# Kernel tuning notes

Hardware: AMD Instinct MI355X
Metric: run time of the kernel (lower is better)

The kernel has to match this reference:

```python
import jax, jax.numpy as jnp
import numpy as np

N = 50000      # total nodes
E = 800000     # total edges (avg degree 16)
D = 64         # in_node_feats = in_edge_feats = out_feats


def setup_inputs() -> dict:
    key = jax.random.key(0)
    ks = jax.random.split(key, 9)
    node_feats = jax.random.normal(ks[0], (N, D), dtype=jnp.float32)
    edge_feats = jax.random.normal(ks[1], (E, D), dtype=jnp.float32)
    src = jax.random.randint(ks[2], (E,), 0, N)
    dst = jax.random.randint(ks[3], (E,), 0, N)
    # in-degree per node (clipped to >=1 to avoid div-by-zero, matching a valid graph)
    deg = jnp.maximum(jax.ops.segment_sum(jnp.ones((E,), jnp.float32), dst, num_segments=N), 1.0)
    degs = deg[:, None]                                   # (N, 1)
    norm = (1.0 / jnp.sqrt(deg[src] * deg[dst]))[:, None]  # (E, 1)
    s = 1.0 / np.sqrt(D)
    Wn = jax.random.uniform(ks[4], (D, D), jnp.float32, -s, s)
    bn = jax.random.uniform(ks[5], (D,), jnp.float32, -s, s)
    We = jax.random.uniform(ks[6], (D, D), jnp.float32, -s, s)
    be = jax.random.uniform(ks[7], (D,), jnp.float32, -s, s)
    res_w = jax.random.normal(ks[8], (1, D), jnp.float32)  # nn.Embedding(1, out_feats).weight
    return {"node_feats": node_feats, "edge_feats": edge_feats, "degs": degs,
            "norm": norm, "src": src, "dst": dst,
            "Wn": Wn, "bn": bn, "We": We, "be": be, "res_w": res_w}


def reference(node_feats, edge_feats, degs, norm, src, dst, Wn, bn, We, be, res_w):
    h = node_feats @ Wn.T + bn                      # (N, D) projected node feats
    ep = edge_feats @ We.T + be                     # (E, D) projected edge feats
    # copy_u gather + relu + norm scale on edges
    m = norm * jax.nn.relu(h[src] + ep)             # (E, D)
    # copy_e + sum scatter-reduction to destination nodes
    agg = jax.ops.segment_sum(m, dst, num_segments=N)  # (N, D)
    # residual branch
    res = jax.nn.relu(h + res_w) / degs             # (N, D), degs broadcasts over D
    return agg + res
```

## Files before the change

kernel.cpp:

```cpp
#include <hip/hip_runtime.h>

#define N_NODES 50000
#define N_EDGES 800000
#define BR 128
#define BRN 64
#define MAXDEG 64
#define NODE_BLOCKS ((N_NODES + BRN - 1) / BRN)
#define ZERO_BLOCKS ((N_NODES + 255) / 256)

using bf16x8 = __attribute__((ext_vector_type(8))) short;
using f32x4  = __attribute__((ext_vector_type(4))) float;

__device__ __forceinline__ unsigned int cvt_pk_bf16(float lo, float hi) {
    unsigned int r;
    asm("v_cvt_pk_bf16_f32 %0, %1, %2" : "=v"(r) : "v"(lo), "v"(hi));
    return r;
}

__device__ __forceinline__ float f4c(const float4 v, int n) {
    switch (n) { case 0: return v.x; case 1: return v.y; case 2: return v.z; default: return v.w; }
}

#define ASWZ(k4, r) (((((r) >> 2) ^ ((k4) & 7)) << 2) | ((r) & 3))

__global__ __launch_bounds__(256) void node_kernel(
    const float* __restrict__ nf, const float* __restrict__ Wn,
    const float* __restrict__ bn, float* __restrict__ h_out,
    const float* __restrict__ We, uint4* __restrict__ Wbe,
    int* __restrict__ cursor) {
    __shared__ float Ast[64][64];
    __shared__ float Ws[64][64];
    const int t = threadIdx.x;
    const int bid = blockIdx.x;

    if (bid >= NODE_BLOCKS) {
        int xb = bid - NODE_BLOCKS;
        if (xb < ZERO_BLOCKS) {
            int i = xb * 256 + t;
            if (i < N_NODES) cursor[i] = 0;
        } else {
#pragma unroll
            for (int i = 0; i < 2; ++i) {
                int task = t + i * 256;
                int frag = task >> 6, lane = task & 63;
                int s = frag >> 2, n = frag & 3;
                int c = 4 * (lane & 15) + n;
                int kb = s * 32 + ((lane >> 4) << 3);
                const float* wp = We + c * 64 + kb;
                float4 a = *(const float4*)wp;
                float4 b = *(const float4*)(wp + 4);
                uint4 o;
                o.x = cvt_pk_bf16(a.x, a.y);
                o.y = cvt_pk_bf16(a.z, a.w);
                o.z = cvt_pk_bf16(b.x, b.y);
                o.w = cvt_pk_bf16(b.z, b.w);
                Wbe[task] = o;
            }
        }
        return;
    }

    const int row0 = bid * BRN;

#pragma unroll
    for (int i = 0; i < 4; ++i) {
        int task = t + i * 256;
        int r = task >> 4;
        int k4 = task & 15;
        int grow = row0 + r;
        float4 v = make_float4(0.f, 0.f, 0.f, 0.f);
        if (grow < N_NODES) v = *(const float4*)(nf + (size_t)grow * 64 + k4 * 4);
        int sc = ASWZ(k4, r);
        Ast[k4 * 4 + 0][sc] = v.x;
        Ast[k4 * 4 + 1][sc] = v.y;
        Ast[k4 * 4 + 2][sc] = v.z;
        Ast[k4 * 4 + 3][sc] = v.w;
    }
#pragma unroll
    for (int i = 0; i < 4; ++i) {
        int task = t + i * 256;
        int c = task & 63;
        int k4 = task >> 6;
        float4 v = *(const float4*)(Wn + c * 64 + k4 * 4);
        Ws[k4 * 4 + 0][c] = v.x;
        Ws[k4 * 4 + 1][c] = v.y;
        Ws[k4 * 4 + 2][c] = v.z;
        Ws[k4 * 4 + 3][c] = v.w;
    }
    __syncthreads();

    const int tx = t & 15, ty = t >> 4;
    const int ca = ty * 4;
    const int cb = tx * 4;

    float acc[4][4];
#pragma unroll
    for (int r = 0; r < 4; ++r)
#pragma unroll
        for (int c = 0; c < 4; ++c) acc[r][c] = 0.f;

#pragma unroll 16
    for (int k = 0; k < 64; ++k) {
        const int f = (k >> 2) & 7;
        float4 w = *(float4*)&Ws[k][cb];
        float4 a = *(float4*)&Ast[k][(ty ^ f) << 2];
        float ar[4] = {a.x, a.y, a.z, a.w};
#pragma unroll
        for (int r = 0; r < 4; ++r) {
            acc[r][0] = fmaf(ar[r], w.x, acc[r][0]);
            acc[r][1] = fmaf(ar[r], w.y, acc[r][1]);
            acc[r][2] = fmaf(ar[r], w.z, acc[r][2]);
            acc[r][3] = fmaf(ar[r], w.w, acc[r][3]);
        }
    }

    float4 b4 = *(const float4*)(bn + cb);
#pragma unroll
    for (int r = 0; r < 4; ++r) {
        int grow = row0 + ca + r;
        if (grow < N_NODES) {
            float4 h4;
            h4.x = acc[r][0] + b4.x;
            h4.y = acc[r][1] + b4.y;
            h4.z = acc[r][2] + b4.z;
            h4.w = acc[r][3] + b4.w;
            *(float4*)(h_out + (size_t)grow * 64 + cb) = h4;
        }
    }
}

__global__ __launch_bounds__(256, 4) void edge_kernel(
    const float* __restrict__ ef, const uint4* __restrict__ Wbe,
    const float* __restrict__ be,
    const int* __restrict__ dst, const float* __restrict__ norm,
    const int* __restrict__ src, int* __restrict__ cursor,
    const float* __restrict__ h, unsigned short* __restrict__ mbuf) {
    __shared__ int slot_l[BR];
    __shared__ float nrm_l[BR];

    const int t = threadIdx.x;
    const int e0 = blockIdx.x * BR;
    const int w = t >> 6, l = t & 63;
    const int l15 = l & 15, lg = l >> 4;
    const int r0base = w * 32;

    if (t < BR) {
        nrm_l[t] = norm[e0 + t];
        int d = dst[e0 + t];
        int rank = atomicAdd(&cursor[d], 1);
        slot_l[t] = (rank < MAXDEG) ? (d * MAXDEG + rank) : -1;
    }

    float4 araw[2][4];
#pragma unroll
    for (int mt = 0; mt < 2; ++mt) {
        const float* rp = ef + (size_t)(e0 + r0base + mt * 16 + l15) * 64 + lg * 8;
        araw[mt][0] = *(const float4*)(rp);
        araw[mt][1] = *(const float4*)(rp + 4);
        araw[mt][2] = *(const float4*)(rp + 32);
        araw[mt][3] = *(const float4*)(rp + 36);
    }
    bf16x8 bfrag[2][4];
#pragma unroll
    for (int s = 0; s < 2; ++s)
#pragma unroll
        for (int n = 0; n < 4; ++n) {
            union { uint4 u; bf16x8 v; } cv;
            cv.u = Wbe[(s * 4 + n) * 64 + l];
            bfrag[s][n] = cv.v;
        }
    float4 hv[2][4];
#pragma unroll
    for (int mt = 0; mt < 2; ++mt)
#pragma unroll
        for (int r = 0; r < 4; ++r) {
            int sn = src[e0 + r0base + mt * 16 + lg * 4 + r];
            hv[mt][r] = *(const float4*)(h + (size_t)sn * 64 + 4 * l15);
        }
    float4 bev4 = *(const float4*)(be + 4 * l15);

    __builtin_amdgcn_sched_barrier(0);

    bf16x8 afrag[2][2];
#pragma unroll
    for (int mt = 0; mt < 2; ++mt)
#pragma unroll
        for (int s = 0; s < 2; ++s) {
            float4 x = araw[mt][s * 2];
            float4 y = araw[mt][s * 2 + 1];
            union { uint4 u; bf16x8 v; } cv;
            cv.u.x = cvt_pk_bf16(x.x, x.y);
            cv.u.y = cvt_pk_bf16(x.z, x.w);
            cv.u.z = cvt_pk_bf16(y.x, y.y);
            cv.u.w = cvt_pk_bf16(y.z, y.w);
            afrag[mt][s] = cv.v;
        }

    f32x4 acc[2][4];
#pragma unroll
    for (int mt = 0; mt < 2; ++mt)
#pragma unroll
        for (int n = 0; n < 4; ++n) acc[mt][n] = (f32x4){0.f, 0.f, 0.f, 0.f};

#pragma unroll
    for (int mt = 0; mt < 2; ++mt)
#pragma unroll
        for (int n = 0; n < 4; ++n)
#pragma unroll
            for (int s = 0; s < 2; ++s)
                acc[mt][n] = __builtin_amdgcn_mfma_f32_16x16x32_bf16(
                    afrag[mt][s], bfrag[s][n], acc[mt][n], 0, 0, 0);

    __syncthreads();

#pragma unroll
    for (int mt = 0; mt < 2; ++mt) {
#pragma unroll
        for (int r = 0; r < 4; ++r) {
            int row = r0base + mt * 16 + lg * 4 + r;
            float nm = nrm_l[row];
            float m0 = nm * fmaxf(f4c(hv[mt][r], 0) + acc[mt][0][r] + bev4.x, 0.f);
            float m1 = nm * fmaxf(f4c(hv[mt][r], 1) + acc[mt][1][r] + bev4.y, 0.f);
            float m2 = nm * fmaxf(f4c(hv[mt][r], 2) + acc[mt][2][r] + bev4.z, 0.f);
            float m3 = nm * fmaxf(f4c(hv[mt][r], 3) + acc[mt][3][r] + bev4.w, 0.f);
            uint2 pk;
            pk.x = cvt_pk_bf16(m0, m1);
            pk.y = cvt_pk_bf16(m2, m3);
            int slot = slot_l[row];
            if (slot >= 0)
                *(uint2*)(mbuf + (size_t)slot * 64 + 4 * l15) = pk;
        }
    }
}

__global__ __launch_bounds__(256, 8) void reduce_kernel(
    const unsigned short* __restrict__ mbuf, const int* __restrict__ cnts,
    const float* __restrict__ h, const float* __restrict__ degs,
    const float* __restrict__ resw, float* __restrict__ out) {
    const int t = threadIdx.x;
    const int n = blockIdx.x * 16 + (t >> 4);
    if (n >= N_NODES) return;
    const int q = t & 15;

    float4 hq = *(const float4*)(h + (size_t)n * 64 + 4 * q);
    float4 rw = *(const float4*)(resw + 4 * q);
    float invd = 1.0f / degs[n];
    int cnt = cnts[n];
    if (cnt > MAXDEG) cnt = MAXDEG;

    const uint2* mp = (const uint2*)mbuf + (size_t)n * MAXDEG * 16 + q;
    float a0 = 0.f, a1 = 0.f, a2 = 0.f, a3 = 0.f;
    float b0 = 0.f, b1 = 0.f, b2 = 0.f, b3 = 0.f;
    int i = 0;
    for (; i + 1 < cnt; i += 2) {
        uint2 va = mp[(size_t)i * 16];
        uint2 vb = mp[(size_t)(i + 1) * 16];
        a0 += __uint_as_float(va.x << 16);
        a1 += __uint_as_float(va.x & 0xffff0000u);
        a2 += __uint_as_float(va.y << 16);
        a3 += __uint_as_float(va.y & 0xffff0000u);
        b0 += __uint_as_float(vb.x << 16);
        b1 += __uint_as_float(vb.x & 0xffff0000u);
        b2 += __uint_as_float(vb.y << 16);
        b3 += __uint_as_float(vb.y & 0xffff0000u);
    }
    if (i < cnt) {
        uint2 v = mp[(size_t)i * 16];
        a0 += __uint_as_float(v.x << 16);
        a1 += __uint_as_float(v.x & 0xffff0000u);
        a2 += __uint_as_float(v.y << 16);
        a3 += __uint_as_float(v.y & 0xffff0000u);
    }
    float4 o;
    o.x = fmaxf(hq.x + rw.x, 0.f) * invd + a0 + b0;
    o.y = fmaxf(hq.y + rw.y, 0.f) * invd + a1 + b1;
    o.z = fmaxf(hq.z + rw.z, 0.f) * invd + a2 + b2;
    o.w = fmaxf(hq.w + rw.w, 0.f) * invd + a3 + b3;
    *(float4*)(out + (size_t)n * 64 + 4 * q) = o;
}

extern "C" void kernel_launch(void* const* d_in, const int* in_sizes, int n_in,
                              void* d_out, int out_size, void* d_ws, size_t ws_size,
                              hipStream_t stream) {
    const float* nf   = (const float*)d_in[0];
    const float* ef   = (const float*)d_in[1];
    const float* degs = (const float*)d_in[2];
    const float* norm = (const float*)d_in[3];
    const int*   src  = (const int*)d_in[4];
    const int*   dst  = (const int*)d_in[5];
    const float* Wn   = (const float*)d_in[6];
    const float* bn   = (const float*)d_in[7];
    const float* We   = (const float*)d_in[8];
    const float* be   = (const float*)d_in[9];
    const float* resw = (const float*)d_in[10];
    float* out = (float*)d_out;

    unsigned short* mbuf = (unsigned short*)d_ws;
    uint4* Wbe = (uint4*)(mbuf + (size_t)N_NODES * MAXDEG * 64);
    float* h   = (float*)(Wbe + 512);
    int* cursor = (int*)(h + (size_t)N_NODES * 64);

    node_kernel<<<NODE_BLOCKS + ZERO_BLOCKS + 1, 256, 0, stream>>>(nf, Wn, bn, h, We, Wbe, cursor);
    edge_kernel<<<N_EDGES / BR, 256, 0, stream>>>(ef, Wbe, be, dst, norm, src, cursor, h, mbuf);
    reduce_kernel<<<(N_NODES + 15) / 16, 256, 0, stream>>>(mbuf, cursor, h, degs, resw, out);
}
```

Baseline: 125.1 us.

## Make edge kernel persistent with grid-stride tiles and nontemporal streaming loads

The edge kernel now launches a fixed grid of 1024 blocks that loop over edge tiles in grid-stride order, instead of one block per 128-edge tile. The weight fragments and bias are loaded once per block, and the slot/norm setup for the next tile is done at the end of each iteration. Edge and node feature loads use nontemporal hints so streaming data does not pollute the cache. In exchange, the explicit sched_barrier is gone and an extra __syncthreads per tile is added. Fewer resident blocks may also leave less memory-level parallelism for latency hiding.

```diff
diff --git a/kernel.cpp b/kernel.cpp
--- a/kernel.cpp
+++ b/kernel.cpp
@@ -5,6 +5,8 @@
 #define BR 128
 #define BRN 64
 #define MAXDEG 64
+#define NTILES (N_EDGES / BR)
+#define GRID_E 1024
 #define NODE_BLOCKS ((N_NODES + BRN - 1) / BRN)
 #define ZERO_BLOCKS ((N_NODES + 255) / 256)
 
@@ -17,8 +19,12 @@
     return r;
 }
 
-__device__ __forceinline__ float f4c(const float4 v, int n) {
+__device__ __forceinline__ float f4c(const f32x4 v, int n) {
     switch (n) { case 0: return v.x; case 1: return v.y; case 2: return v.z; default: return v.w; }
+}
+
+__device__ __forceinline__ f32x4 ntload4(const float* p) {
+    return __builtin_nontemporal_load((const f32x4*)p);
 }
 
 #define ASWZ(k4, r) (((((r) >> 2) ^ ((k4) & 7)) << 2) | ((r) & 3))
@@ -68,8 +74,9 @@
         int r = task >> 4;
         int k4 = task & 15;
         int grow = row0 + r;
-        float4 v = make_float4(0.f, 0.f, 0.f, 0.f);
-        if (grow < N_NODES) v = *(const float4*)(nf + (size_t)grow * 64 + k4 * 4);
+        f32x4 v = (f32x4){0.f, 0.f, 0.f, 0.f};
+        if (grow < N_NODES)
+            v = ntload4(nf + (size_t)grow * 64 + k4 * 4);
         int sc = ASWZ(k4, r);
         Ast[k4 * 4 + 0][sc] = v.x;
         Ast[k4 * 4 + 1][sc] = v.y;
@@ -139,27 +146,10 @@
     __shared__ float nrm_l[BR];
 
     const int t = threadIdx.x;
-    const int e0 = blockIdx.x * BR;
     const int w = t >> 6, l = t & 63;
     const int l15 = l & 15, lg = l >> 4;
     const int r0base = w * 32;
 
-    if (t < BR) {
-        nrm_l[t] = norm[e0 + t];
-        int d = dst[e0 + t];
-        int rank = atomicAdd(&cursor[d], 1);
-        slot_l[t] = (rank < MAXDEG) ? (d * MAXDEG + rank) : -1;
-    }
-
-    float4 araw[2][4];
-#pragma unroll
-    for (int mt = 0; mt < 2; ++mt) {
-        const float* rp = ef + (size_t)(e0 + r0base + mt * 16 + l15) * 64 + lg * 8;
-        araw[mt][0] = *(const float4*)(rp);
-        araw[mt][1] = *(const float4*)(rp + 4);
-        araw[mt][2] = *(const float4*)(rp + 32);
-        araw[mt][3] = *(const float4*)(rp + 36);
-    }
     bf16x8 bfrag[2][4];
 #pragma unroll
     for (int s = 0; s < 2; ++s)
@@ -169,66 +159,99 @@
             cv.u = Wbe[(s * 4 + n) * 64 + l];
             bfrag[s][n] = cv.v;
         }
-    float4 hv[2][4];
-#pragma unroll
-    for (int mt = 0; mt < 2; ++mt)
-#pragma unroll
-        for (int r = 0; r < 4; ++r) {
-            int sn = src[e0 + r0base + mt * 16 + lg * 4 + r];
-            hv[mt][r] = *(const float4*)(h + (size_t)sn * 64 + 4 * l15);
-        }
-    float4 bev4 = *(const float4*)(be + 4 * l15);
-
-    __builtin_amdgcn_sched_barrier(0);
-
-    bf16x8 afrag[2][2];
-#pragma unroll
-    for (int mt = 0; mt < 2; ++mt)
-#pragma unroll
-        for (int s = 0; s < 2; ++s) {
-            float4 x = araw[mt][s * 2];
-            float4 y = araw[mt][s * 2 + 1];
-            union { uint4 u; bf16x8 v; } cv;
-            cv.u.x = cvt_pk_bf16(x.x, x.y);
-            cv.u.y = cvt_pk_bf16(x.z, x.w);
-            cv.u.z = cvt_pk_bf16(y.x, y.y);
-            cv.u.w = cvt_pk_bf16(y.z, y.w);
-            afrag[mt][s] = cv.v;
-        }
-
-    f32x4 acc[2][4];
-#pragma unroll
-    for (int mt = 0; mt < 2; ++mt)
-#pragma unroll
-        for (int n = 0; n < 4; ++n) acc[mt][n] = (f32x4){0.f, 0.f, 0.f, 0.f};
-
-#pragma unroll
-    for (int mt = 0; mt < 2; ++mt)
-#pragma unroll
-        for (int n = 0; n < 4; ++n)
-#pragma unroll
-            for (int s = 0; s < 2; ++s)
-                acc[mt][n] = __builtin_amdgcn_mfma_f32_16x16x32_bf16(
-                    afrag[mt][s], bfrag[s][n], acc[mt][n], 0, 0, 0);
-
-    __syncthreads();
-
-#pragma unroll
-    for (int mt = 0; mt < 2; ++mt) {
-#pragma unroll
-        for (int r = 0; r < 4; ++r) {
-            int row = r0base + mt * 16 + lg * 4 + r;
-            float nm = nrm_l[row];
-            float m0 = nm * fmaxf(f4c(hv[mt][r], 0) + acc[mt][0][r] + bev4.x, 0.f);
-            float m1 = nm * fmaxf(f4c(hv[mt][r], 1) + acc[mt][1][r] + bev4.y, 0.f);
-            float m2 = nm * fmaxf(f4c(hv[mt][r], 2) + acc[mt][2][r] + bev4.z, 0.f);
-            float m3 = nm * fmaxf(f4c(hv[mt][r], 3) + acc[mt][3][r] + bev4.w, 0.f);
-            uint2 pk;
-            pk.x = cvt_pk_bf16(m0, m1);
-            pk.y = cvt_pk_bf16(m2, m3);
-            int slot = slot_l[row];
-            if (slot >= 0)
-                *(uint2*)(mbuf + (size_t)slot * 64 + 4 * l15) = pk;
+    f32x4 bev4 = *(const f32x4*)(be + 4 * l15);
+
+    {
+        int tile0 = blockIdx.x;
+        if (tile0 < NTILES && t < BR) {
+            int e0 = tile0 * BR;
+            nrm_l[t] = norm[e0 + t];
+            int d = dst[e0 + t];
+            int rank = atomicAdd(&cursor[d], 1);
+            slot_l[t] = (rank < MAXDEG) ? (d * MAXDEG + rank) : -1;
+        }
+    }
+
+    for (int tile = blockIdx.x; tile < NTILES; tile += GRID_E) {
+        const int e0 = tile * BR;
+
+        f32x4 araw[2][4];
+#pragma unroll
+        for (int mt = 0; mt < 2; ++mt) {
+            const float* rp = ef + (size_t)(e0 + r0base + mt * 16 + l15) * 64 + lg * 8;
+            araw[mt][0] = ntload4(rp);
+            araw[mt][1] = ntload4(rp + 4);
+            araw[mt][2] = ntload4(rp + 32);
+            araw[mt][3] = ntload4(rp + 36);
+        }
+        f32x4 hv[2][4];
+#pragma unroll
+        for (int mt = 0; mt < 2; ++mt)
+#pragma unroll
+            for (int r = 0; r < 4; ++r) {
+                int sn = src[e0 + r0base + mt * 16 + lg * 4 + r];
+                hv[mt][r] = *(const f32x4*)(h + (size_t)sn * 64 + 4 * l15);
+            }
+
+        bf16x8 afrag[2][2];
+#pragma unroll
+        for (int mt = 0; mt < 2; ++mt)
+#pragma unroll
+            for (int s = 0; s < 2; ++s) {
+                f32x4 x = araw[mt][s * 2];
+                f32x4 y = araw[mt][s * 2 + 1];
+                union { uint4 u; bf16x8 v; } cv;
+                cv.u.x = cvt_pk_bf16(x.x, x.y);
+                cv.u.y = cvt_pk_bf16(x.z, x.w);
+                cv.u.z = cvt_pk_bf16(y.x, y.y);
+                cv.u.w = cvt_pk_bf16(y.z, y.w);
+                afrag[mt][s] = cv.v;
+            }
+
+        f32x4 acc[2][4];
+#pragma unroll
+        for (int mt = 0; mt < 2; ++mt)
+#pragma unroll
+            for (int n = 0; n < 4; ++n) acc[mt][n] = (f32x4){0.f, 0.f, 0.f, 0.f};
+
+#pragma unroll
+        for (int mt = 0; mt < 2; ++mt)
+#pragma unroll
+            for (int n = 0; n < 4; ++n)
+#pragma unroll
+                for (int s = 0; s < 2; ++s)
+                    acc[mt][n] = __builtin_amdgcn_mfma_f32_16x16x32_bf16(
+                        afrag[mt][s], bfrag[s][n], acc[mt][n], 0, 0, 0);
+
+        __syncthreads();
+
+#pragma unroll
+        for (int mt = 0; mt < 2; ++mt) {
+#pragma unroll
+            for (int r = 0; r < 4; ++r) {
+                int row = r0base + mt * 16 + lg * 4 + r;
+                float nm = nrm_l[row];
+                float m0 = nm * fmaxf(f4c(hv[mt][r], 0) + acc[mt][0][r] + bev4.x, 0.f);
+                float m1 = nm * fmaxf(f4c(hv[mt][r], 1) + acc[mt][1][r] + bev4.y, 0.f);
+                float m2 = nm * fmaxf(f4c(hv[mt][r], 2) + acc[mt][2][r] + bev4.z, 0.f);
+                float m3 = nm * fmaxf(f4c(hv[mt][r], 3) + acc[mt][3][r] + bev4.w, 0.f);
+                uint2 pk;
+                pk.x = cvt_pk_bf16(m0, m1);
+                pk.y = cvt_pk_bf16(m2, m3);
+                int slot = slot_l[row];
+                if (slot >= 0)
+                    *(uint2*)(mbuf + (size_t)slot * 64 + 4 * l15) = pk;
+            }
+        }
+        __syncthreads();
+
+        int ntile = tile + GRID_E;
+        if (ntile < NTILES && t < BR) {
+            int e0n = ntile * BR;
+            nrm_l[t] = norm[e0n + t];
+            int d = dst[e0n + t];
+            int rank = atomicAdd(&cursor[d], 1);
+            slot_l[t] = (rank < MAXDEG) ? (d * MAXDEG + rank) : -1;
         }
     }
 }
@@ -301,6 +324,6 @@
     int* cursor = (int*)(h + (size_t)N_NODES * 64);
 
     node_kernel<<<NODE_BLOCKS + ZERO_BLOCKS + 1, 256, 0, stream>>>(nf, Wn, bn, h, We, Wbe, cursor);
-    edge_kernel<<<N_EDGES / BR, 256, 0, stream>>>(ef, Wbe, be, dst, norm, src, cursor, h, mbuf);
+    edge_kernel<<<GRID_E, 256, 0, stream>>>(ef, Wbe, be, dst, norm, src, cursor, h, mbuf);
     reduce_kernel<<<(N_NODES + 15) / 16, 256, 0, stream>>>(mbuf, cursor, h, degs, resw, out);
 }
```

Result: slower. 128.0 us (+2.4%).
